# Kernel tuning notes

Measured on AMD Instinct MI355X. Metric: run time of the kernel, lower is better.

## Reference

```python
import jax, jax.numpy as jnp
import numpy as np

INV_SCALE = 8.0  # math.sqrt(64) in the original source


def setup_inputs() -> dict:
    key = jax.random.key(0)
    kq, kk, kv = jax.random.split(key, 3)
    B, S, D = 8, 2048, 128
    q1 = jax.random.normal(kq, (B, S, D), dtype=jnp.float32)
    k1 = jax.random.normal(kk, (B, S, D), dtype=jnp.float32)
    v1 = jax.random.normal(kv, (B, S, D), dtype=jnp.float32)
    return {"q1": q1, "k1": k1, "v1": v1}


def reference(q1, k1, v1):
    # qk = q1 @ k1^T over last two dims  -> [B, S, S]
    scaled_qk = jnp.einsum("bsd,btd->bst", q1, k1) / INV_SCALE
    # original computes softmax(scaled_qk) but never uses it (dead code);
    # dropout is applied to scaled_qk and is identity in eval mode.
    out = jnp.einsum("bst,btd->bsd", scaled_qk, v1)  # [B, S, D]
    return out
```

## Files before the change

### kernel.cpp

```cpp
#include <hip/hip_runtime.h>
#include <hip/hip_bf16.h>


#define B 8
#define S 2048
#define D 128
#define CH 8
#define SC 256

typedef __attribute__((ext_vector_type(8))) short short8;
typedef __attribute__((ext_vector_type(4))) float f32x4;

static __device__ __forceinline__ short f2bf(float f) {
    __hip_bfloat16 h = __float2bfloat16(f);
    union { __hip_bfloat16 h; short s; } u; u.h = h;
    return u.s;
}
static __device__ __forceinline__ float bf2f(unsigned short s) {
    union { unsigned u; float f; } x; x.u = ((unsigned)s) << 16;
    return x.f;
}

__global__ __launch_bounds__(512) void k1_ktv(
    const float* __restrict__ K, const float* __restrict__ V,
    unsigned short* __restrict__ P)
{
    int blk = blockIdx.x;
    int b = blk >> 4, rem = blk & 15;
    int ch = rem >> 1, h = rem & 1;
    const float* Kb = K + ((size_t)b * S + (size_t)ch * SC) * D;
    const float* Vb = V + ((size_t)b * S + (size_t)ch * SC) * D;

    int tid = threadIdx.x;
    int w = tid >> 6, l = tid & 63;
    int lr = l & 15, lg = l >> 4;
    int dr0 = h * 64 + (w >> 2) * 32;
    int cc0 = (w & 3) * 32;

    f32x4 acc[2][2];
#pragma unroll
    for (int i = 0; i < 2; i++)
#pragma unroll
        for (int j = 0; j < 2; j++) acc[i][j] = (f32x4)0.f;

    for (int ks = 0; ks < 8; ++ks) {
        int sb = ks * 32 + lg * 8;
        short8 af[2], bv[2];
#pragma unroll
        for (int fi = 0; fi < 2; ++fi) {
            const float* kp = Kb + (size_t)sb * D + dr0 + fi * 16 + lr;
            float t[8];
#pragma unroll
            for (int i = 0; i < 8; ++i) t[i] = kp[(size_t)i * D];
            short8 s8;
#pragma unroll
            for (int i = 0; i < 8; ++i) s8[i] = f2bf(t[i]);
            af[fi] = s8;
        }
#pragma unroll
        for (int fj = 0; fj < 2; ++fj) {
            const float* vp = Vb + (size_t)sb * D + cc0 + fj * 16 + lr;
            float t[8];
#pragma unroll
            for (int i = 0; i < 8; ++i) t[i] = vp[(size_t)i * D];
            short8 s8;
#pragma unroll
            for (int i = 0; i < 8; ++i) s8[i] = f2bf(t[i]);
            bv[fj] = s8;
        }
#pragma unroll
        for (int fi = 0; fi < 2; ++fi)
#pragma unroll
            for (int fj = 0; fj < 2; ++fj)
                acc[fi][fj] = __builtin_amdgcn_mfma_f32_16x16x32_bf16(
                    af[fi], bv[fj], acc[fi][fj], 0, 0, 0);
    }

    unsigned short* Pb = P + (size_t)(b * CH + ch) * D * D;
#pragma unroll
    for (int fi = 0; fi < 2; ++fi)
#pragma unroll
        for (int fj = 0; fj < 2; ++fj)
#pragma unroll
            for (int j = 0; j < 4; ++j) {
                int row = dr0 + fi * 16 + lg * 4 + j;
                int col = cc0 + fj * 16 + lr;
                Pb[row * D + col] = (unsigned short)f2bf(acc[fi][fj][j]);
            }
}

__global__ __launch_bounds__(256) void k2_rqm(
    const float* __restrict__ Q, const unsigned short* __restrict__ P,
    float* __restrict__ Out)
{
    __shared__ unsigned short MT[D * D];

    int blk = blockIdx.x;
    int b = blk >> 5, t = blk & 31;
    int tid = threadIdx.x;

    int cblk = tid & 15, dblk = tid >> 4;
    int c0 = cblk * 8, d0 = dblk * 8;
    const unsigned short* Pb = P + (size_t)(b * CH) * D * D;

    float m[8][8];
#pragma unroll
    for (int j = 0; j < 8; ++j)
#pragma unroll
        for (int i = 0; i < 8; ++i) m[j][i] = 0.f;

#pragma unroll
    for (int cc = 0; cc < CH; ++cc) {
#pragma unroll
        for (int j = 0; j < 8; ++j) {
            short8 pv = *(const short8*)(Pb + (size_t)cc * D * D + (d0 + j) * D + c0);
#pragma unroll
            for (int i = 0; i < 8; ++i)
                m[j][i] += bf2f((unsigned short)pv[i]);
        }
    }

    char* mt = (char*)MT;
#pragma unroll
    for (int i = 0; i < 8; ++i) {
        int c = c0 + i;
        short8 sv;
#pragma unroll
        for (int j = 0; j < 8; ++j) sv[j] = f2bf(m[j][i] * 0.125f);
        int X = ((c & 7) ^ (cblk & 7)) & 7;
        int byte = (c * 256 + 2 * d0) ^ (X << 4);
        *(short8*)(mt + byte) = sv;
    }
    __syncthreads();

    int w = tid >> 6, l = tid & 63;
    int lr = l & 15, lg = l >> 4;
    int r0 = t * 64 + w * 16;

    const float* Qb = Q + ((size_t)b * S + r0) * D;

    f32x4 acc[8];
#pragma unroll
    for (int j = 0; j < 8; ++j) acc[j] = (f32x4)0.f;

#pragma unroll
    for (int ks = 0; ks < 4; ++ks) {
        int k0 = ks * 32 + lg * 8;
        const float* qp = Qb + (size_t)lr * D + k0;
        float4 q0 = *(const float4*)qp;
        float4 q1 = *(const float4*)(qp + 4);
        short8 a;
        a[0] = f2bf(q0.x); a[1] = f2bf(q0.y); a[2] = f2bf(q0.z); a[3] = f2bf(q0.w);
        a[4] = f2bf(q1.x); a[5] = f2bf(q1.y); a[6] = f2bf(q1.z); a[7] = f2bf(q1.w);
#pragma unroll
        for (int fj = 0; fj < 8; ++fj) {
            int c = fj * 16 + lr;
            int X = ((c & 7) ^ ((c >> 3) & 7)) & 7;
            int byte = (c * 256 + 2 * k0) ^ (X << 4);
            short8 bb = *(const short8*)(mt + byte);
            acc[fj] = __builtin_amdgcn_mfma_f32_16x16x32_bf16(a, bb, acc[fj], 0, 0, 0);
        }
    }

    float* Ob = Out + ((size_t)b * S + r0) * D;
#pragma unroll
    for (int fj = 0; fj < 8; ++fj)
#pragma unroll
        for (int j = 0; j < 4; ++j)
            Ob[(size_t)(lg * 4 + j) * D + fj * 16 + lr] = acc[fj][j];
}

extern "C" void kernel_launch(void* const* d_in, const int* in_sizes, int n_in,
                              void* d_out, int out_size, void* d_ws, size_t ws_size,
                              hipStream_t stream)
{
    const float* q = (const float*)d_in[0];
    const float* k = (const float*)d_in[1];
    const float* v = (const float*)d_in[2];
    float* out = (float*)d_out;

    unsigned short* P = (unsigned short*)d_ws;

    k1_ktv<<<B * CH * 2, 512, 0, stream>>>(k, v, P);
    k2_rqm<<<B * 32, 256, 0, stream>>>(q, P, out);
}
```

Before: 23.75 us.

## Stage K and V through swizzled LDS with coalesced vector loads in KᵀV kernel

The KᵀV partial-product kernel used to build MFMA fragments from strided scalar global loads, one float per row. It now loads K and V tiles with coalesced float4 loads, converts them to bf16, and writes them transposed into XOR-swizzled shared memory in 64-row stages. MFMA operands are then read from LDS, and each wave tile is reshaped to 16x64. The aim is to cut uncoalesced global traffic and redundant loads, at the cost of extra LDS traffic and barriers per stage.

```diff
diff --git a/kernel.cpp b/kernel.cpp
--- a/kernel.cpp
+++ b/kernel.cpp
@@ -7,6 +7,7 @@
 #define D 128
 #define CH 8
 #define SC 256
+#define STG 64
 
 typedef __attribute__((ext_vector_type(8))) short short8;
 typedef __attribute__((ext_vector_type(4))) float f32x4;
@@ -19,6 +20,9 @@
 static __device__ __forceinline__ float bf2f(unsigned short s) {
     union { unsigned u; float f; } x; x.u = ((unsigned)s) << 16;
     return x.f;
+}
+static __device__ __forceinline__ int swz(int d, int byte) {
+    return byte ^ (((d >> 2) & 7) << 4);
 }
 
 __global__ __launch_bounds__(512) void k1_ktv(
@@ -26,67 +30,88 @@
     unsigned short* __restrict__ P)
 {
     int blk = blockIdx.x;
-    int b = blk >> 4, rem = blk & 15;
-    int ch = rem >> 1, h = rem & 1;
-    const float* Kb = K + ((size_t)b * S + (size_t)ch * SC) * D;
+    int b = blk >> 4;
+    int ch = (blk >> 1) & 7;
+    int h  = blk & 1;
+    const float* Kb = K + ((size_t)b * S + (size_t)ch * SC) * D + h * 64;
     const float* Vb = V + ((size_t)b * S + (size_t)ch * SC) * D;
+
+    __shared__ unsigned short Kt[64 * STG];
+    __shared__ unsigned short Vt[128 * STG];
 
     int tid = threadIdx.x;
     int w = tid >> 6, l = tid & 63;
     int lr = l & 15, lg = l >> 4;
-    int dr0 = h * 64 + (w >> 2) * 32;
-    int cc0 = (w & 3) * 32;
-
-    f32x4 acc[2][2];
-#pragma unroll
-    for (int i = 0; i < 2; i++)
-#pragma unroll
-        for (int j = 0; j < 2; j++) acc[i][j] = (f32x4)0.f;
-
-    for (int ks = 0; ks < 8; ++ks) {
-        int sb = ks * 32 + lg * 8;
-        short8 af[2], bv[2];
-#pragma unroll
-        for (int fi = 0; fi < 2; ++fi) {
-            const float* kp = Kb + (size_t)sb * D + dr0 + fi * 16 + lr;
-            float t[8];
-#pragma unroll
-            for (int i = 0; i < 8; ++i) t[i] = kp[(size_t)i * D];
-            short8 s8;
-#pragma unroll
-            for (int i = 0; i < 8; ++i) s8[i] = f2bf(t[i]);
-            af[fi] = s8;
-        }
-#pragma unroll
-        for (int fj = 0; fj < 2; ++fj) {
-            const float* vp = Vb + (size_t)sb * D + cc0 + fj * 16 + lr;
-            float t[8];
-#pragma unroll
-            for (int i = 0; i < 8; ++i) t[i] = vp[(size_t)i * D];
-            short8 s8;
-#pragma unroll
-            for (int i = 0; i < 8; ++i) s8[i] = f2bf(t[i]);
-            bv[fj] = s8;
-        }
-#pragma unroll
-        for (int fi = 0; fi < 2; ++fi)
-#pragma unroll
-            for (int fj = 0; fj < 2; ++fj)
-                acc[fi][fj] = __builtin_amdgcn_mfma_f32_16x16x32_bf16(
-                    af[fi], bv[fj], acc[fi][fj], 0, 0, 0);
+    int ds0 = (w & 3) * 16;
+    int cc0 = (w >> 2) * 64;
+
+    int kd0 = 4 * (tid & 15), ks0 = 2 * (tid >> 4);
+    int vd0 = 4 * (tid & 31), vs0 = 4 * (tid >> 5);
+
+    f32x4 acc[4];
+#pragma unroll
+    for (int j = 0; j < 4; ++j) acc[j] = (f32x4)0.f;
+
+    char* ktb = (char*)Kt;
+    char* vtb = (char*)Vt;
+
+#pragma unroll
+    for (int st = 0; st < SC / STG; ++st) {
+        f32x4 kv[2], vv[4];
+        const float* Kg = Kb + (size_t)(st * STG) * D;
+        const float* Vg = Vb + (size_t)(st * STG) * D;
+#pragma unroll
+        for (int r = 0; r < 2; ++r)
+            kv[r] = *(const f32x4*)(Kg + (size_t)(ks0 + r) * D + kd0);
+#pragma unroll
+        for (int r = 0; r < 4; ++r)
+            vv[r] = *(const f32x4*)(Vg + (size_t)(vs0 + r) * D + vd0);
+
+        if (st > 0) __syncthreads();
+
+#pragma unroll
+        for (int j = 0; j < 4; ++j) {
+            int d = kd0 + j;
+            unsigned pv = (unsigned)(unsigned short)f2bf(kv[0][j]) |
+                          ((unsigned)(unsigned short)f2bf(kv[1][j]) << 16);
+            *(unsigned*)(ktb + swz(d, (d << 7) + (ks0 << 1))) = pv;
+        }
+#pragma unroll
+        for (int j = 0; j < 4; ++j) {
+            int d = vd0 + j;
+            uint2 qv;
+            qv.x = (unsigned)(unsigned short)f2bf(vv[0][j]) |
+                   ((unsigned)(unsigned short)f2bf(vv[1][j]) << 16);
+            qv.y = (unsigned)(unsigned short)f2bf(vv[2][j]) |
+                   ((unsigned)(unsigned short)f2bf(vv[3][j]) << 16);
+            *(uint2*)(vtb + swz(d, (d << 7) + (vs0 << 1))) = qv;
+        }
+        __syncthreads();
+
+#pragma unroll
+        for (int ks = 0; ks < 2; ++ks) {
+            int sb = ks * 32 + lg * 8;
+            int da = ds0 + lr;
+            short8 af = *(const short8*)(ktb + swz(da, (da << 7) + (sb << 1)));
+#pragma unroll
+            for (int fj = 0; fj < 4; ++fj) {
+                int c = cc0 + fj * 16 + lr;
+                short8 bv = *(const short8*)(vtb + swz(c, (c << 7) + (sb << 1)));
+                acc[fj] = __builtin_amdgcn_mfma_f32_16x16x32_bf16(
+                    af, bv, acc[fj], 0, 0, 0);
+            }
+        }
     }
 
     unsigned short* Pb = P + (size_t)(b * CH + ch) * D * D;
 #pragma unroll
-    for (int fi = 0; fi < 2; ++fi)
-#pragma unroll
-        for (int fj = 0; fj < 2; ++fj)
-#pragma unroll
-            for (int j = 0; j < 4; ++j) {
-                int row = dr0 + fi * 16 + lg * 4 + j;
-                int col = cc0 + fj * 16 + lr;
-                Pb[row * D + col] = (unsigned short)f2bf(acc[fi][fj][j]);
-            }
+    for (int fj = 0; fj < 4; ++fj)
+#pragma unroll
+        for (int j = 0; j < 4; ++j) {
+            int row = h * 64 + ds0 + lg * 4 + j;
+            int col = cc0 + fj * 16 + lr;
+            Pb[row * D + col] = (unsigned short)f2bf(acc[fj][j]);
+        }
 }
 
 __global__ __launch_bounds__(256) void k2_rqm(
```

After: 23.99 us. About the same (+1.0%).
